# Kernel optimization log

Measured on AMD Instinct MI355X. Metric: run time of the kernel, lower is better.

## Reference

```python
import jax, jax.numpy as jnp
import numpy as np

ALPHA = 1.0   # init alpha=1 -> temporal (TDI) term has zero weight
GAMMA = 0.01  # soft-min temperature
INF = 1e9     # finite stand-in for +inf boundary of the DP matrix


def setup_inputs() -> dict:
    key = jax.random.key(0)
    k1, k2 = jax.random.split(key)
    B, N, F = 64, 512, 1
    return {
        "input": jax.random.normal(k1, (B, N, F), dtype=jnp.float32),
        "target": jax.random.normal(k2, (B, N, F), dtype=jnp.float32),
    }


def _soft_dtw(D, gamma):
    """Batched soft-DTW value via anti-diagonal wavefront scan.

    D: (B, n, n) cost matrix. Returns (B,) soft-DTW values R[n, n].
    Recursion: R[i,j] = D[i-1,j-1] + softmin_gamma(R[i-1,j-1], R[i-1,j], R[i,j-1]).
    """
    B, n, _ = D.shape
    ii = jnp.arange(n + 1)           # row index i of diagonal entries
    ic = jnp.clip(ii - 1, 0, n - 1)  # clipped cost-row index (masked below)
    inf_row = jnp.full((B, n + 1), INF, D.dtype)
    diag_d0 = inf_row.at[:, 0].set(0.0)  # R[0,0]=0, rest inf
    diag_d1 = inf_row                    # R[1,0]=R[0,1]=inf
    pad_col = jnp.full((B, 1), INF, D.dtype)

    def step(carry, d):
        r2, r1 = carry  # diagonals d-2, d-1, indexed by i in [0, n]
        jj = d - ii
        jc = jnp.clip(jj - 1, 0, n - 1)
        dvals = D[:, ic, jc]  # (B, n+1) costs along diagonal d
        r2s = jnp.concatenate([pad_col, r2[:, :-1]], axis=1)  # R[i-1, j-1]
        r1s = jnp.concatenate([pad_col, r1[:, :-1]], axis=1)  # R[i-1, j]
        # softmin_gamma(a,b,c) = -gamma * logsumexp(-[a,b,c]/gamma)
        cand = jnp.stack([-r2s, -r1s, -r1], axis=0) / gamma
        smin = -gamma * jax.nn.logsumexp(cand, axis=0)
        valid = (ii >= 1) & (ii <= n) & (jj >= 1) & (jj <= n)
        new = jnp.where(valid[None, :], dvals + smin, INF)
        return (r1, new), None

    (_, last), _ = jax.lax.scan(step, (diag_d0, diag_d1), jnp.arange(2, 2 * n + 1))
    return last[:, n]  # R[n, n] per batch element


def reference(input, target):
    # derivative DILATE: operate on first differences of the series
    dx = input[:, 1:, :] - input[:, :-1, :]   # (B, n, F), n = N-1
    dy = target[:, 1:, :] - target[:, :-1, :]
    # pairwise squared-Euclidean cost D[b, i, j] = ||dy_i - dx_j||^2
    D = jnp.sum((dy[:, :, None, :] - dx[:, None, :, :]) ** 2, axis=-1)
    loss_shape = jnp.mean(_soft_dtw(D, GAMMA))
    # DILATE = alpha * loss_shape + (1 - alpha) * loss_temporal; alpha == 1 here,
    # so the TDI (temporal) term has zero weight and is omitted.
    return ALPHA * loss_shape
```

## Files before the change

kernel.cpp:

```cpp
#include <hip/hip_runtime.h>
#include <math.h>


#define INF_F 1000000000.0f

typedef float v4f __attribute__((ext_vector_type(4)));

__device__ __forceinline__ float dpp_shr1_inj(float x, float oldv){
  int r = __builtin_amdgcn_update_dpp(__float_as_int(oldv), __float_as_int(x),
                                      0x138 , 0xf, 0xf, false);
  return __int_as_float(r);
}
#define PINF(v) asm volatile("" : "+v"(v))

#define LOADX(P, B) { const int _b = (B); \
  P##0  = dxe[_b];     P##1  = dxe[_b+1];  P##2  = dxe[_b+2];  P##3  = dxe[_b+3]; \
  P##4  = dxe[_b+4];   P##5  = dxe[_b+5];  P##6  = dxe[_b+6];  P##7  = dxe[_b+7]; \
  P##8  = dxe[_b+8];   P##9  = dxe[_b+9];  P##10 = dxe[_b+10]; P##11 = dxe[_b+11]; \
  P##12 = dxe[_b+12];  P##13 = dxe[_b+13]; P##14 = dxe[_b+14]; P##15 = dxe[_b+15]; }

#define PINX(P) { PINF(P##0); PINF(P##1); PINF(P##2); PINF(P##3); PINF(P##4); \
  PINF(P##5); PINF(P##6); PINF(P##7); PINF(P##8); PINF(P##9); PINF(P##10); \
  PINF(P##11); PINF(P##12); PINF(P##13); PINF(P##14); PINF(P##15); }

#define STEP(K, MB, XW) { \
  float sh1 = dpp_shr1_inj(r1, (MB)); \
  float m_  = fminf(fminf(SH, sh1), r1); \
  float u_  = dy - (XW); \
  float nv  = fmaf(u_, u_, m_); \
  pb##K = nv; \
  if ((K) == 12) { if (cc == 63) ans = nv; } \
  SH = sh1; r1 = nv; }

#define CHUNK(C, XU, XP) { \
  const int cc = (C); \
  if (w > 0) { \
    while (__hip_atomic_load(&flagz[w-1], __ATOMIC_ACQUIRE, \
                             __HIP_MEMORY_SCOPE_WORKGROUP) <= cc) {} \
    const v4f* Mr = (const v4f*)&Mbx[w][16*cc]; \
    q0 = Mr[0]; q1 = Mr[1]; q2 = Mr[2]; q3 = Mr[3]; m16v = Mbx[w][16*cc+16]; \
    PINF(q0); PINF(q1); PINF(q2); PINF(q3); PINF(m16v); \
  } \
  PINX(XU); \
  LOADX(XP, dxb + 16*(cc+1)); \
  asm volatile("" ::: "memory"); \
  STEP(0,  q0.y,  XU##0 ) \
  STEP(1,  q0.z,  XU##1 ) \
  STEP(2,  q0.w,  XU##2 ) \
  STEP(3,  q1.x,  XU##3 ) \
  STEP(4,  q1.y,  XU##4 ) \
  STEP(5,  q1.z,  XU##5 ) \
  STEP(6,  q1.w,  XU##6 ) \
  STEP(7,  q2.x,  XU##7 ) \
  STEP(8,  q2.y,  XU##8 ) \
  STEP(9,  q2.z,  XU##9 ) \
  STEP(10, q2.w,  XU##10) \
  STEP(11, q3.x,  XU##11) \
  STEP(12, q3.y,  XU##12) \
  STEP(13, q3.z,  XU##13) \
  STEP(14, q3.w,  XU##14) \
  STEP(15, m16v,  XU##15) \
  if (w < 7) { \
    if (lane == 63) { \
      float2* Pd = (float2*)&Mbx[w+1][16*cc+2]; \
      Pd[0] = make_float2(pb0,  pb1);  Pd[1] = make_float2(pb2,  pb3); \
      Pd[2] = make_float2(pb4,  pb5);  Pd[3] = make_float2(pb6,  pb7); \
      Pd[4] = make_float2(pb8,  pb9);  Pd[5] = make_float2(pb10, pb11); \
      Pd[6] = make_float2(pb12, pb13); Pd[7] = make_float2(pb14, pb15); \
    } \
    __hip_atomic_store(&flagz[w], cc+1, __ATOMIC_RELEASE, \
                       __HIP_MEMORY_SCOPE_WORKGROUP); \
  } }

__global__ __launch_bounds__(512)
void sdtw_kernel(const float* __restrict__ input,
                 const float* __restrict__ target,
                 float* __restrict__ out) {
  const int b = blockIdx.x;
  const int t = threadIdx.x;
  const int w = t >> 6;
  const int lane = t & 63;

  __shared__ float dxe[1560];
  __shared__ __align__(16) float Mbx[8][1040];
  __shared__ int flagz[8];

  const float* __restrict__ inp = input + b * 512;
  const float* __restrict__ tgt = target + b * 512;

  for (int idx = t; idx < 1560; idx += 512) {
    float v = 0.0f;
    if (idx >= 513 && idx <= 1023) v = inp[idx - 512] - inp[idx - 513];
    dxe[idx] = v;
  }
  for (int k2 = t; k2 < 8 * 1040; k2 += 512) (&Mbx[0][0])[k2] = INF_F;
  if (t < 8) flagz[t] = 0;

  float dy = (t >= 1) ? (tgt[t] - tgt[t - 1]) : 0.0f;

  float r1 = INF_F;
  float r2i = (t == 0) ? 0.0f : INF_F;
  float SH  = dpp_shr1_inj(r2i, INF_F);

  v4f q0 = {INF_F, INF_F, INF_F, INF_F};
  v4f q1 = q0, q2 = q0, q3 = q0;
  float m16v = INF_F;
  float pb0, pb1, pb2, pb3, pb4, pb5, pb6, pb7;
  float pb8, pb9, pb10, pb11, pb12, pb13, pb14, pb15;
  float xa0, xa1, xa2, xa3, xa4, xa5, xa6, xa7;
  float xa8, xa9, xa10, xa11, xa12, xa13, xa14, xa15;
  float xb0, xb1, xb2, xb3, xb4, xb5, xb6, xb7;
  float xb8, xb9, xb10, xb11, xb12, xb13, xb14, xb15;

  const int dxb = 514 - t;
  float ans = INF_F;

  __syncthreads();

  LOADX(xa, dxb);

#pragma unroll 1
  for (int c = 0; c < 64; c += 2) {
    CHUNK(c,     xa, xb)
    CHUNK(c + 1, xb, xa)
  }

  if (w == 7 && lane == 63) {
    atomicAdd(out, ans * (1.0f / 64.0f));
  }
}

extern "C" void kernel_launch(void* const* d_in, const int* in_sizes, int n_in,
                              void* d_out, int out_size, void* d_ws, size_t ws_size,
                              hipStream_t stream) {
  const float* input  = (const float*)d_in[0];
  const float* target = (const float*)d_in[1];
  float* out = (float*)d_out;

  hipMemsetAsync(out, 0, sizeof(float), stream);
  sdtw_kernel<<<64, 512, 0, stream>>>(input, target, out);
}
```

Baseline: 94.58 us.

## Double chunk size and stream dx through DPP shift with readlane injection

Each wave now processes 32 anti-diagonals per chunk instead of 16, which halves the number of inter-wave flag handoffs and LDS boundary exchanges. The per-lane x values are no longer loaded as 16 registers from LDS each chunk. A single register is shifted across lanes with DPP, and a readlane injects the next x value into lane 0. The cost is a longer pipeline fill, since downstream waves wait for larger chunks, plus an extra readlane and DPP on every step of the serial dependency chain.

```diff
diff --git a/kernel.cpp b/kernel.cpp
--- a/kernel.cpp
+++ b/kernel.cpp
@@ -13,64 +13,16 @@
 }
 #define PINF(v) asm volatile("" : "+v"(v))
 
-#define LOADX(P, B) { const int _b = (B); \
-  P##0  = dxe[_b];     P##1  = dxe[_b+1];  P##2  = dxe[_b+2];  P##3  = dxe[_b+3]; \
-  P##4  = dxe[_b+4];   P##5  = dxe[_b+5];  P##6  = dxe[_b+6];  P##7  = dxe[_b+7]; \
-  P##8  = dxe[_b+8];   P##9  = dxe[_b+9];  P##10 = dxe[_b+10]; P##11 = dxe[_b+11]; \
-  P##12 = dxe[_b+12];  P##13 = dxe[_b+13]; P##14 = dxe[_b+14]; P##15 = dxe[_b+15]; }
-
-#define PINX(P) { PINF(P##0); PINF(P##1); PINF(P##2); PINF(P##3); PINF(P##4); \
-  PINF(P##5); PINF(P##6); PINF(P##7); PINF(P##8); PINF(P##9); PINF(P##10); \
-  PINF(P##11); PINF(P##12); PINF(P##13); PINF(P##14); PINF(P##15); }
-
-#define STEP(K, MB, XW) { \
+#define STEP(K, MB) { \
   float sh1 = dpp_shr1_inj(r1, (MB)); \
+  float u_  = dy - XW; \
+  int   sv  = __builtin_amdgcn_readlane(__float_as_int(wv), (K)); \
+  XW = dpp_shr1_inj(XW, __int_as_float(sv)); \
   float m_  = fminf(fminf(SH, sh1), r1); \
-  float u_  = dy - (XW); \
   float nv  = fmaf(u_, u_, m_); \
   pb##K = nv; \
-  if ((K) == 12) { if (cc == 63) ans = nv; } \
+  if ((K) == 28) { if (cc == 31) ans = nv; } \
   SH = sh1; r1 = nv; }
-
-#define CHUNK(C, XU, XP) { \
-  const int cc = (C); \
-  if (w > 0) { \
-    while (__hip_atomic_load(&flagz[w-1], __ATOMIC_ACQUIRE, \
-                             __HIP_MEMORY_SCOPE_WORKGROUP) <= cc) {} \
-    const v4f* Mr = (const v4f*)&Mbx[w][16*cc]; \
-    q0 = Mr[0]; q1 = Mr[1]; q2 = Mr[2]; q3 = Mr[3]; m16v = Mbx[w][16*cc+16]; \
-    PINF(q0); PINF(q1); PINF(q2); PINF(q3); PINF(m16v); \
-  } \
-  PINX(XU); \
-  LOADX(XP, dxb + 16*(cc+1)); \
-  asm volatile("" ::: "memory"); \
-  STEP(0,  q0.y,  XU##0 ) \
-  STEP(1,  q0.z,  XU##1 ) \
-  STEP(2,  q0.w,  XU##2 ) \
-  STEP(3,  q1.x,  XU##3 ) \
-  STEP(4,  q1.y,  XU##4 ) \
-  STEP(5,  q1.z,  XU##5 ) \
-  STEP(6,  q1.w,  XU##6 ) \
-  STEP(7,  q2.x,  XU##7 ) \
-  STEP(8,  q2.y,  XU##8 ) \
-  STEP(9,  q2.z,  XU##9 ) \
-  STEP(10, q2.w,  XU##10) \
-  STEP(11, q3.x,  XU##11) \
-  STEP(12, q3.y,  XU##12) \
-  STEP(13, q3.z,  XU##13) \
-  STEP(14, q3.w,  XU##14) \
-  STEP(15, m16v,  XU##15) \
-  if (w < 7) { \
-    if (lane == 63) { \
-      float2* Pd = (float2*)&Mbx[w+1][16*cc+2]; \
-      Pd[0] = make_float2(pb0,  pb1);  Pd[1] = make_float2(pb2,  pb3); \
-      Pd[2] = make_float2(pb4,  pb5);  Pd[3] = make_float2(pb6,  pb7); \
-      Pd[4] = make_float2(pb8,  pb9);  Pd[5] = make_float2(pb10, pb11); \
-      Pd[6] = make_float2(pb12, pb13); Pd[7] = make_float2(pb14, pb15); \
-    } \
-    __hip_atomic_store(&flagz[w], cc+1, __ATOMIC_RELEASE, \
-                       __HIP_MEMORY_SCOPE_WORKGROUP); \
-  } }
 
 __global__ __launch_bounds__(512)
 void sdtw_kernel(const float* __restrict__ input,
@@ -81,14 +33,14 @@
   const int w = t >> 6;
   const int lane = t & 63;
 
-  __shared__ float dxe[1560];
+  __shared__ float dxe[1608];
   __shared__ __align__(16) float Mbx[8][1040];
   __shared__ int flagz[8];
 
   const float* __restrict__ inp = input + b * 512;
   const float* __restrict__ tgt = target + b * 512;
 
-  for (int idx = t; idx < 1560; idx += 512) {
+  for (int idx = t; idx < 1608; idx += 512) {
     float v = 0.0f;
     if (idx >= 513 && idx <= 1023) v = inp[idx - 512] - inp[idx - 513];
     dxe[idx] = v;
@@ -103,26 +55,65 @@
   float SH  = dpp_shr1_inj(r2i, INF_F);
 
   v4f q0 = {INF_F, INF_F, INF_F, INF_F};
-  v4f q1 = q0, q2 = q0, q3 = q0;
-  float m16v = INF_F;
-  float pb0, pb1, pb2, pb3, pb4, pb5, pb6, pb7;
-  float pb8, pb9, pb10, pb11, pb12, pb13, pb14, pb15;
-  float xa0, xa1, xa2, xa3, xa4, xa5, xa6, xa7;
-  float xa8, xa9, xa10, xa11, xa12, xa13, xa14, xa15;
-  float xb0, xb1, xb2, xb3, xb4, xb5, xb6, xb7;
-  float xb8, xb9, xb10, xb11, xb12, xb13, xb14, xb15;
+  v4f q1 = q0, q2 = q0, q3 = q0, q4 = q0, q5 = q0, q6 = q0, q7 = q0;
+  float m32v = INF_F;
+  float pb0,  pb1,  pb2,  pb3,  pb4,  pb5,  pb6,  pb7;
+  float pb8,  pb9,  pb10, pb11, pb12, pb13, pb14, pb15;
+  float pb16, pb17, pb18, pb19, pb20, pb21, pb22, pb23;
+  float pb24, pb25, pb26, pb27, pb28, pb29, pb30, pb31;
 
-  const int dxb = 514 - t;
   float ans = INF_F;
 
   __syncthreads();
 
-  LOADX(xa, dxb);
+  float XW = dxe[514 - t];
+  const float* dxw = &dxe[515 - 64 * w];
+  float wv  = dxw[lane];
+  float wvn;
+  PINF(XW); PINF(wv);
 
 #pragma unroll 1
-  for (int c = 0; c < 64; c += 2) {
-    CHUNK(c,     xa, xb)
-    CHUNK(c + 1, xb, xa)
+  for (int c = 0; c < 32; ++c) {
+    const int cc = c;
+    if (w > 0) {
+      while (__hip_atomic_load(&flagz[w - 1], __ATOMIC_ACQUIRE,
+                               __HIP_MEMORY_SCOPE_WORKGROUP) <= cc) {}
+      const v4f* Mr = (const v4f*)&Mbx[w][32 * cc];
+      q0 = Mr[0]; q1 = Mr[1]; q2 = Mr[2]; q3 = Mr[3];
+      q4 = Mr[4]; q5 = Mr[5]; q6 = Mr[6]; q7 = Mr[7];
+      m32v = Mbx[w][32 * cc + 32];
+      PINF(q0); PINF(q1); PINF(q2); PINF(q3);
+      PINF(q4); PINF(q5); PINF(q6); PINF(q7); PINF(m32v);
+    }
+    wvn = dxw[32 * (cc + 1) + lane];
+    asm volatile("" ::: "memory");
+
+    STEP(0,  q0.y ) STEP(1,  q0.z ) STEP(2,  q0.w ) STEP(3,  q1.x )
+    STEP(4,  q1.y ) STEP(5,  q1.z ) STEP(6,  q1.w ) STEP(7,  q2.x )
+    STEP(8,  q2.y ) STEP(9,  q2.z ) STEP(10, q2.w ) STEP(11, q3.x )
+    STEP(12, q3.y ) STEP(13, q3.z ) STEP(14, q3.w ) STEP(15, q4.x )
+    STEP(16, q4.y ) STEP(17, q4.z ) STEP(18, q4.w ) STEP(19, q5.x )
+    STEP(20, q5.y ) STEP(21, q5.z ) STEP(22, q5.w ) STEP(23, q6.x )
+    STEP(24, q6.y ) STEP(25, q6.z ) STEP(26, q6.w ) STEP(27, q7.x )
+    STEP(28, q7.y ) STEP(29, q7.z ) STEP(30, q7.w ) STEP(31, m32v)
+
+    if (w < 7) {
+      if (lane == 63) {
+        float2* Pd = (float2*)&Mbx[w + 1][32 * cc + 2];
+        Pd[0]  = make_float2(pb0,  pb1);  Pd[1]  = make_float2(pb2,  pb3);
+        Pd[2]  = make_float2(pb4,  pb5);  Pd[3]  = make_float2(pb6,  pb7);
+        Pd[4]  = make_float2(pb8,  pb9);  Pd[5]  = make_float2(pb10, pb11);
+        Pd[6]  = make_float2(pb12, pb13); Pd[7]  = make_float2(pb14, pb15);
+        Pd[8]  = make_float2(pb16, pb17); Pd[9]  = make_float2(pb18, pb19);
+        Pd[10] = make_float2(pb20, pb21); Pd[11] = make_float2(pb22, pb23);
+        Pd[12] = make_float2(pb24, pb25); Pd[13] = make_float2(pb26, pb27);
+        Pd[14] = make_float2(pb28, pb29); Pd[15] = make_float2(pb30, pb31);
+      }
+      __hip_atomic_store(&flagz[w], cc + 1, __ATOMIC_RELEASE,
+                         __HIP_MEMORY_SCOPE_WORKGROUP);
+    }
+    wv = wvn;
+    PINF(wv);
   }
 
   if (w == 7 && lane == 63) {
```

Measured after the change: 99.92 us. 5.6% more time.
